# Optimization experiments

Measured on AMD Instinct MI355X. Metric: run time of the kernel, lower is better.

Reference implementation:

```python
import jax, jax.numpy as jnp
import numpy as np
from jax.scipy.special import logsumexp

L, B, T = 512, 512, 128


def setup_inputs() -> dict:
    key = jax.random.key(0)
    k0, k1, k2, k3, k4 = jax.random.split(key, 5)
    emissions = jax.random.normal(k0, (L, B, T), dtype=jnp.float32)
    tags = jax.random.randint(k1, (L, B), 0, T)
    mask = jnp.ones((L, B), dtype=bool)
    u = lambda k, s: jax.random.uniform(k, s, jnp.float32, -0.1, 0.1)
    return {
        "emissions": emissions,
        "tags": tags,
        "mask": mask,
        "start_transitions": u(k2, (T,)),
        "end_transitions": u(k3, (T,)),
        "transitions": u(k4, (T, T)),
    }


def reference(emissions, tags, mask, start_transitions, end_transitions, transitions):
    # emissions: (L, B, T) float; tags: (L, B) int; mask: (L, B) bool
    seq_len, batch, n_tag = emissions.shape

    # ---- numerator: score of the gold tag sequence (summed over batch) ----
    # per-step emission score at the gold tag
    step_scores = jnp.take_along_axis(emissions, tags[:, :, None], axis=2)[:, :, 0]  # (L, B)
    # transition score tags[i-1] -> tags[i] for i >= 1
    trans_scores = transitions[tags[:-1], tags[1:]]  # (L-1, B)
    scores = step_scores.at[1:].add(trans_scores)
    log_numerator = jnp.sum(jnp.where(mask, scores, jnp.float32(0.0)))
    ends = mask.sum(axis=0) - 1  # (B,) last valid index per sequence
    log_numerator += start_transitions[tags[0]].sum()
    last_tags = jnp.take_along_axis(tags, ends[None, :], axis=0)[0]  # (B,)
    log_numerator += end_transitions[last_tags].sum()

    # ---- denominator: log partition via forward algorithm (lax.scan over time) ----
    alpha0 = start_transitions + emissions[0]  # (B, T)

    def step(alpha, xs):
        emit_i, mask_i = xs  # (B, T), (B,)
        # scores[b, s, t] = alpha[b, s] + transitions[s, t] + emit_i[b, t]
        scores = alpha[:, :, None] + transitions[None, :, :] + emit_i[:, None, :]
        new_alpha = logsumexp(scores, axis=1)  # (B, T)
        alpha = jnp.where(mask_i[:, None], new_alpha, alpha)
        return alpha, None

    alpha, _ = jax.lax.scan(step, alpha0, (emissions[1:], mask[1:]))
    log_denominator = logsumexp(alpha + end_transitions, axis=1).sum()

    return (log_denominator - log_numerator) / batch
```

## Files before the change

### kernel.cpp

```cpp
#include <hip/hip_runtime.h>

#define L_SEQ 512
#define BATCH 512
#define NTAG  128
#define LOG2E 1.44269504088896340736f
#define LN2_D 0.69314718055994530942

typedef _Float16 h2 __attribute__((ext_vector_type(2)));
typedef _Float16 h8 __attribute__((ext_vector_type(8)));


__global__ void k_init(const float* __restrict__ trans, h2* __restrict__ ctp,
                       int* __restrict__ counter) {
    int g = blockIdx.x * blockDim.x + threadIdx.x;
    if (g < NTAG * 64) {
        int j = g >> 6, t = g & 63;
        h2 v;
        v[0] = (_Float16)__expf(trans[(2 * t)     * NTAG + j]);
        v[1] = (_Float16)__expf(trans[(2 * t + 1) * NTAG + j]);
        ctp[g] = v;
    }
    if (g == 0) *counter = 0;
}

#define Q16(F) F(0) F(1) F(2) F(3) F(4) F(5) F(6) F(7) \
               F(8) F(9) F(10) F(11) F(12) F(13) F(14) F(15)

#define DECL_C(n) h8 c##n = colp[n];

#define DOTG(n) { h8 qv = q8[n]; \
  s0 = __builtin_amdgcn_fdot2(__builtin_shufflevector(qv, qv, 0, 1), \
                              __builtin_shufflevector(c##n, c##n, 0, 1), s0, false); \
  s1 = __builtin_amdgcn_fdot2(__builtin_shufflevector(qv, qv, 2, 3), \
                              __builtin_shufflevector(c##n, c##n, 2, 3), s1, false); \
  s2 = __builtin_amdgcn_fdot2(__builtin_shufflevector(qv, qv, 4, 5), \
                              __builtin_shufflevector(c##n, c##n, 4, 5), s2, false); \
  s3 = __builtin_amdgcn_fdot2(__builtin_shufflevector(qv, qv, 6, 7), \
                              __builtin_shufflevector(c##n, c##n, 6, 7), s3, false); }

__global__ void __launch_bounds__(128, 1)
k_main(const float* __restrict__ emissions,
       const int* __restrict__ tags,
       const float* __restrict__ start_t,
       const float* __restrict__ end_t,
       const float* __restrict__ trans,
       const h2* __restrict__ ctp,
       float* __restrict__ ws_val,
       int* __restrict__ counter,
       float* __restrict__ out) {
    const int b = blockIdx.x;
    const int j = threadIdx.x;
    const int wave = j >> 6;
    const int lane = j & 63;

    __shared__ __align__(16) _Float16 q_h[2][136];
    __shared__ float D_sh[2];
    __shared__ float red_sh[2];
    __shared__ int   s_last;

    float num = 0.f;
    #pragma unroll
    for (int l = j; l < L_SEQ; l += 128) {
        int tag = tags[l * BATCH + b];
        float sc = emissions[((size_t)l * BATCH + b) * NTAG + tag];
        if (l > 0) {
            int prev = tags[(l - 1) * BATCH + b];
            sc += trans[prev * NTAG + tag];
        } else {
            sc += start_t[tag];
        }
        if (l == L_SEQ - 1) sc += end_t[tag];
        num += sc;
    }
    #pragma unroll
    for (int off = 32; off; off >>= 1) num += __shfl_xor(num, off, 64);
    if (lane == 0) red_sh[wave] = num;

    const h8* colp = (const h8*)(ctp + (size_t)j * 64);
    Q16(DECL_C)

    __syncthreads();
    const float num_b = red_sh[0] + red_sh[1];

    const float ee = __expf(end_t[j]);
    float alpha0 = start_t[j] + emissions[(size_t)b * NTAG + j];
    float q_own = exp2f(alpha0 * LOG2E);
    double C = 0.0;

    float m0 = alpha0;
    #pragma unroll
    for (int off = 32; off; off >>= 1) m0 = fmaxf(m0, __shfl_xor(m0, off, 64));
    __syncthreads();
    if (lane == 0) red_sh[wave] = m0;
    __syncthreads();
    float D_stash = fmaxf(red_sh[0], red_sh[1]) * LOG2E + 13.5f;

    const size_t STRIDE = (size_t)BATCH * NTAG;
    const float* em_base = emissions + (size_t)b * NTAG + j;
    float em_cur = em_base[1 * STRIDE];
    float em_n1  = em_base[2 * STRIDE];
    float em_n2  = em_base[3 * STRIDE];

    for (int l = 1; l < L_SEQ; ++l) {
        const int p = l & 1;
        q_h[p][j] = (_Float16)fminf(q_own, 60000.f);
        if (j == 0) D_sh[p] = D_stash;
        int pf = l + 3; if (pf > L_SEQ - 1) pf = L_SEQ - 1;
        float em_pf = em_base[(size_t)pf * STRIDE];

        __syncthreads();
        const h8* q8 = (const h8*)q_h[p];
        float D_f = D_sh[p];

        float s0 = 0.f, s1 = 0.f, s2 = 0.f, s3 = 0.f;
        Q16(DOTG)

        float S = (s0 + s1) + (s2 + s3);
        if (j == 0)
            D_stash = fmaf(0.5f, __log2f(fmaxf(S, 1e-30f)),
                           fmaf(0.3f, D_f, 6.5f));
        q_own = S * exp2f(fmaf(em_cur, LOG2E, -D_f));
        C += (double)D_f * LN2_D;

        em_cur = em_n1; em_n1 = em_n2; em_n2 = em_pf;
    }

    float wv = q_own * ee;
    #pragma unroll
    for (int off = 32; off; off >>= 1) wv += __shfl_xor(wv, off, 64);
    __syncthreads();
    if (lane == 0) red_sh[wave] = wv;
    __syncthreads();
    float tot = red_sh[0] + red_sh[1];
    float val = (float)(C + (double)__logf(tot)) - num_b;

    if (j == 0) {
        __hip_atomic_store(&ws_val[b], val, __ATOMIC_RELAXED, __HIP_MEMORY_SCOPE_AGENT);
        __threadfence();
        int old = atomicAdd(counter, 1);
        s_last = (old == (int)gridDim.x - 1) ? 1 : 0;
    }
    __syncthreads();
    if (s_last) {
        __threadfence();
        float acc = 0.f;
        #pragma unroll
        for (int t = j; t < BATCH; t += 128)
            acc += __hip_atomic_load(&ws_val[t], __ATOMIC_RELAXED, __HIP_MEMORY_SCOPE_AGENT);
        #pragma unroll
        for (int off = 32; off; off >>= 1) acc += __shfl_xor(acc, off, 64);
        if (lane == 0) red_sh[wave] = acc;
        __syncthreads();
        if (j == 0) out[0] = (red_sh[0] + red_sh[1]) / (float)BATCH;
    }
}

extern "C" void kernel_launch(void* const* d_in, const int* in_sizes, int n_in,
                              void* d_out, int out_size, void* d_ws, size_t ws_size,
                              hipStream_t stream) {
    const float* emissions = (const float*)d_in[0];
    const int*   tags      = (const int*)d_in[1];
    const float* start_t   = (const float*)d_in[3];
    const float* end_t     = (const float*)d_in[4];
    const float* trans     = (const float*)d_in[5];

    char*  wsb     = (char*)d_ws;
    h2*    ctp     = (h2*)wsb;
    float* ws_val  = (float*)(wsb + 32768);
    int*   counter = (int*)(wsb + 32768 + 2048);
    float* out     = (float*)d_out;

    k_init<<<(NTAG * 64 + 255) / 256, 256, 0, stream>>>(trans, ctp, counter);
    k_main<<<BATCH, NTAG, 0, stream>>>(emissions, tags, start_t, end_t, trans, ctp,
                                       ws_val, counter, out);
}
```

Measured before the change: 438.6 us.

## Split each tag's transition dot product across four threads per block

Raises the block from 128 to 512 threads and gives each tag a quad of threads. Each thread holds a quarter of the transition column and does 16 fdot2 instead of 64, then the quad combines its partial sums with two cross-lane shuffles. This shortens the per-step critical path of the serial forward recurrence, which is latency-bound with only 2 waves per block. The cost is redundant emission loads and exp work in each quad, two extra shuffles per step, and reductions over 8 waves instead of 2.

After: 439.2 us. About the same (+0.1%).

```diff
diff --git a/kernel.cpp b/kernel.cpp
--- a/kernel.cpp
+++ b/kernel.cpp
@@ -3,6 +3,7 @@
 #define L_SEQ 512
 #define BATCH 512
 #define NTAG  128
+#define NTHR  512
 #define LOG2E 1.44269504088896340736f
 #define LN2_D 0.69314718055994530942
 
@@ -23,22 +24,17 @@
     if (g == 0) *counter = 0;
 }
 
-#define Q16(F) F(0) F(1) F(2) F(3) F(4) F(5) F(6) F(7) \
-               F(8) F(9) F(10) F(11) F(12) F(13) F(14) F(15)
+#define DOTG(cn, n) { h8 qv = q8[qbase + n]; \
+  s0 = __builtin_amdgcn_fdot2(__builtin_shufflevector(qv, qv, 0, 1), \
+                              __builtin_shufflevector(cn, cn, 0, 1), s0, false); \
+  s1 = __builtin_amdgcn_fdot2(__builtin_shufflevector(qv, qv, 2, 3), \
+                              __builtin_shufflevector(cn, cn, 2, 3), s1, false); \
+  s2 = __builtin_amdgcn_fdot2(__builtin_shufflevector(qv, qv, 4, 5), \
+                              __builtin_shufflevector(cn, cn, 4, 5), s2, false); \
+  s3 = __builtin_amdgcn_fdot2(__builtin_shufflevector(qv, qv, 6, 7), \
+                              __builtin_shufflevector(cn, cn, 6, 7), s3, false); }
 
-#define DECL_C(n) h8 c##n = colp[n];
-
-#define DOTG(n) { h8 qv = q8[n]; \
-  s0 = __builtin_amdgcn_fdot2(__builtin_shufflevector(qv, qv, 0, 1), \
-                              __builtin_shufflevector(c##n, c##n, 0, 1), s0, false); \
-  s1 = __builtin_amdgcn_fdot2(__builtin_shufflevector(qv, qv, 2, 3), \
-                              __builtin_shufflevector(c##n, c##n, 2, 3), s1, false); \
-  s2 = __builtin_amdgcn_fdot2(__builtin_shufflevector(qv, qv, 4, 5), \
-                              __builtin_shufflevector(c##n, c##n, 4, 5), s2, false); \
-  s3 = __builtin_amdgcn_fdot2(__builtin_shufflevector(qv, qv, 6, 7), \
-                              __builtin_shufflevector(c##n, c##n, 6, 7), s3, false); }
-
-__global__ void __launch_bounds__(128, 1)
+__global__ void __launch_bounds__(NTHR, 4)
 k_main(const float* __restrict__ emissions,
        const int* __restrict__ tags,
        const float* __restrict__ start_t,
@@ -48,19 +44,21 @@
        float* __restrict__ ws_val,
        int* __restrict__ counter,
        float* __restrict__ out) {
-    const int b = blockIdx.x;
-    const int j = threadIdx.x;
-    const int wave = j >> 6;
-    const int lane = j & 63;
+    const int b    = blockIdx.x;
+    const int t    = threadIdx.x;
+    const int j    = t >> 2;
+    const int qh   = t & 3;
+    const int wave = t >> 6;
+    const int lane = t & 63;
 
-    __shared__ __align__(16) _Float16 q_h[2][136];
+    __shared__ __align__(16) _Float16 q_h[2][NTAG];
     __shared__ float D_sh[2];
-    __shared__ float red_sh[2];
+    __shared__ float red_sh[8];
     __shared__ int   s_last;
 
-    float num = 0.f;
-    #pragma unroll
-    for (int l = j; l < L_SEQ; l += 128) {
+    float num;
+    {
+        const int l = t;
         int tag = tags[l * BATCH + b];
         float sc = emissions[((size_t)l * BATCH + b) * NTAG + tag];
         if (l > 0) {
@@ -70,17 +68,23 @@
             sc += start_t[tag];
         }
         if (l == L_SEQ - 1) sc += end_t[tag];
-        num += sc;
+        num = sc;
     }
     #pragma unroll
     for (int off = 32; off; off >>= 1) num += __shfl_xor(num, off, 64);
     if (lane == 0) red_sh[wave] = num;
 
+    const int qbase = qh * 4;
     const h8* colp = (const h8*)(ctp + (size_t)j * 64);
-    Q16(DECL_C)
+    h8 c0 = colp[qbase + 0];
+    h8 c1 = colp[qbase + 1];
+    h8 c2 = colp[qbase + 2];
+    h8 c3 = colp[qbase + 3];
 
     __syncthreads();
-    const float num_b = red_sh[0] + red_sh[1];
+    float num_b = 0.f;
+    #pragma unroll
+    for (int w = 0; w < 8; ++w) num_b += red_sh[w];
 
     const float ee = __expf(end_t[j]);
     float alpha0 = start_t[j] + emissions[(size_t)b * NTAG + j];
@@ -93,7 +97,10 @@
     __syncthreads();
     if (lane == 0) red_sh[wave] = m0;
     __syncthreads();
-    float D_stash = fmaxf(red_sh[0], red_sh[1]) * LOG2E + 13.5f;
+    float mx = red_sh[0];
+    #pragma unroll
+    for (int w = 1; w < 8; ++w) mx = fmaxf(mx, red_sh[w]);
+    float D_stash = mx * LOG2E + 13.5f;
 
     const size_t STRIDE = (size_t)BATCH * NTAG;
     const float* em_base = emissions + (size_t)b * NTAG + j;
@@ -103,8 +110,8 @@
 
     for (int l = 1; l < L_SEQ; ++l) {
         const int p = l & 1;
-        q_h[p][j] = (_Float16)fminf(q_own, 60000.f);
-        if (j == 0) D_sh[p] = D_stash;
+        if (qh == 0) q_h[p][j] = (_Float16)fminf(q_own, 60000.f);
+        if (t == 0)  D_sh[p] = D_stash;
         int pf = l + 3; if (pf > L_SEQ - 1) pf = L_SEQ - 1;
         float em_pf = em_base[(size_t)pf * STRIDE];
 
@@ -113,10 +120,13 @@
         float D_f = D_sh[p];
 
         float s0 = 0.f, s1 = 0.f, s2 = 0.f, s3 = 0.f;
-        Q16(DOTG)
+        DOTG(c0, 0) DOTG(c1, 1) DOTG(c2, 2) DOTG(c3, 3)
 
         float S = (s0 + s1) + (s2 + s3);
-        if (j == 0)
+        S += __shfl_xor(S, 1, 64);
+        S += __shfl_xor(S, 2, 64);
+
+        if (t == 0)
             D_stash = fmaf(0.5f, __log2f(fmaxf(S, 1e-30f)),
                            fmaf(0.3f, D_f, 6.5f));
         q_own = S * exp2f(fmaf(em_cur, LOG2E, -D_f));
@@ -125,16 +135,18 @@
         em_cur = em_n1; em_n1 = em_n2; em_n2 = em_pf;
     }
 
-    float wv = q_own * ee;
+    float wv = (qh == 0) ? q_own * ee : 0.f;
     #pragma unroll
     for (int off = 32; off; off >>= 1) wv += __shfl_xor(wv, off, 64);
     __syncthreads();
     if (lane == 0) red_sh[wave] = wv;
     __syncthreads();
-    float tot = red_sh[0] + red_sh[1];
+    float tot = 0.f;
+    #pragma unroll
+    for (int w = 0; w < 8; ++w) tot += red_sh[w];
     float val = (float)(C + (double)__logf(tot)) - num_b;
 
-    if (j == 0) {
+    if (t == 0) {
         __hip_atomic_store(&ws_val[b], val, __ATOMIC_RELAXED, __HIP_MEMORY_SCOPE_AGENT);
         __threadfence();
         int old = atomicAdd(counter, 1);
@@ -143,15 +155,18 @@
     __syncthreads();
     if (s_last) {
         __threadfence();
-        float acc = 0.f;
-        #pragma unroll
-        for (int t = j; t < BATCH; t += 128)
-            acc += __hip_atomic_load(&ws_val[t], __ATOMIC_RELAXED, __HIP_MEMORY_SCOPE_AGENT);
+        float acc = __hip_atomic_load(&ws_val[t], __ATOMIC_RELAXED,
+                                      __HIP_MEMORY_SCOPE_AGENT);
         #pragma unroll
         for (int off = 32; off; off >>= 1) acc += __shfl_xor(acc, off, 64);
         if (lane == 0) red_sh[wave] = acc;
         __syncthreads();
-        if (j == 0) out[0] = (red_sh[0] + red_sh[1]) / (float)BATCH;
+        if (t == 0) {
+            float a = 0.f;
+            #pragma unroll
+            for (int w = 0; w < 8; ++w) a += red_sh[w];
+            out[0] = a / (float)BATCH;
+        }
     }
 }
 
@@ -171,6 +186,6 @@
     float* out     = (float*)d_out;
 
     k_init<<<(NTAG * 64 + 255) / 256, 256, 0, stream>>>(trans, ctp, counter);
-    k_main<<<BATCH, NTAG, 0, stream>>>(emissions, tags, start_t, end_t, trans, ctp,
+    k_main<<<BATCH, NTHR, 0, stream>>>(emissions, tags, start_t, end_t, trans, ctp,
                                        ws_val, counter, out);
 }
```

## Run forward recursion in a single wave using readlane broadcast instead of LDS

Applied to the files above, without the earlier changes.

Each batch sequence now runs in one 64-lane wavefront that owns two tags per lane, and the transition matrix is repacked so lane j holds the columns for tags j and j+64. The per-step alpha vector is packed as fp16 pairs and broadcast with readlane instead of going through shared memory. This removes the per-step __syncthreads and LDS traffic, and the scale factor D is computed redundantly on every lane rather than passed through shared memory. In exchange each lane does twice the dot-product work and holds twice the transition registers, and there are half as many threads per CU.

Result: no change. 435.8 us (-0.6%).

```diff
diff --git a/kernel.cpp b/kernel.cpp
--- a/kernel.cpp
+++ b/kernel.cpp
@@ -16,8 +16,8 @@
     if (g < NTAG * 64) {
         int j = g >> 6, t = g & 63;
         h2 v;
-        v[0] = (_Float16)__expf(trans[(2 * t)     * NTAG + j]);
-        v[1] = (_Float16)__expf(trans[(2 * t + 1) * NTAG + j]);
+        v[0] = (_Float16)__expf(trans[t * NTAG + j]);
+        v[1] = (_Float16)__expf(trans[(t + 64) * NTAG + j]);
         ctp[g] = v;
     }
     if (g == 0) *counter = 0;
@@ -26,19 +26,27 @@
 #define Q16(F) F(0) F(1) F(2) F(3) F(4) F(5) F(6) F(7) \
                F(8) F(9) F(10) F(11) F(12) F(13) F(14) F(15)
 
-#define DECL_C(n) h8 c##n = colp[n];
+#define DECL_C(n) h8 cA##n = colA[n]; h8 cB##n = colB[n];
 
-#define DOTG(n) { h8 qv = q8[n]; \
-  s0 = __builtin_amdgcn_fdot2(__builtin_shufflevector(qv, qv, 0, 1), \
-                              __builtin_shufflevector(c##n, c##n, 0, 1), s0, false); \
-  s1 = __builtin_amdgcn_fdot2(__builtin_shufflevector(qv, qv, 2, 3), \
-                              __builtin_shufflevector(c##n, c##n, 2, 3), s1, false); \
-  s2 = __builtin_amdgcn_fdot2(__builtin_shufflevector(qv, qv, 4, 5), \
-                              __builtin_shufflevector(c##n, c##n, 4, 5), s2, false); \
-  s3 = __builtin_amdgcn_fdot2(__builtin_shufflevector(qv, qv, 6, 7), \
-                              __builtin_shufflevector(c##n, c##n, 6, 7), s3, false); }
+#define CHUNK(c) { \
+    int r0 = __builtin_amdgcn_readlane(qpk_i, 4*(c)+0); \
+    int r1 = __builtin_amdgcn_readlane(qpk_i, 4*(c)+1); \
+    int r2 = __builtin_amdgcn_readlane(qpk_i, 4*(c)+2); \
+    int r3 = __builtin_amdgcn_readlane(qpk_i, 4*(c)+3); \
+    h2 b0 = __builtin_bit_cast(h2, r0); \
+    h2 b1 = __builtin_bit_cast(h2, r1); \
+    h2 b2 = __builtin_bit_cast(h2, r2); \
+    h2 b3 = __builtin_bit_cast(h2, r3); \
+    sA0 = __builtin_amdgcn_fdot2(b0, __builtin_shufflevector(cA##c, cA##c, 0, 1), sA0, false); \
+    sA1 = __builtin_amdgcn_fdot2(b1, __builtin_shufflevector(cA##c, cA##c, 2, 3), sA1, false); \
+    sA2 = __builtin_amdgcn_fdot2(b2, __builtin_shufflevector(cA##c, cA##c, 4, 5), sA2, false); \
+    sA3 = __builtin_amdgcn_fdot2(b3, __builtin_shufflevector(cA##c, cA##c, 6, 7), sA3, false); \
+    sB0 = __builtin_amdgcn_fdot2(b0, __builtin_shufflevector(cB##c, cB##c, 0, 1), sB0, false); \
+    sB1 = __builtin_amdgcn_fdot2(b1, __builtin_shufflevector(cB##c, cB##c, 2, 3), sB1, false); \
+    sB2 = __builtin_amdgcn_fdot2(b2, __builtin_shufflevector(cB##c, cB##c, 4, 5), sB2, false); \
+    sB3 = __builtin_amdgcn_fdot2(b3, __builtin_shufflevector(cB##c, cB##c, 6, 7), sB3, false); }
 
-__global__ void __launch_bounds__(128, 1)
+__global__ void __launch_bounds__(64, 1)
 k_main(const float* __restrict__ emissions,
        const int* __restrict__ tags,
        const float* __restrict__ start_t,
@@ -48,19 +56,14 @@
        float* __restrict__ ws_val,
        int* __restrict__ counter,
        float* __restrict__ out) {
-    const int b = blockIdx.x;
-    const int j = threadIdx.x;
-    const int wave = j >> 6;
-    const int lane = j & 63;
-
-    __shared__ __align__(16) _Float16 q_h[2][136];
-    __shared__ float D_sh[2];
-    __shared__ float red_sh[2];
-    __shared__ int   s_last;
+    const int b    = blockIdx.x;
+    const int lane = threadIdx.x;
+    const int j    = lane;
 
     float num = 0.f;
     #pragma unroll
-    for (int l = j; l < L_SEQ; l += 128) {
+    for (int k = 0; k < L_SEQ / 64; ++k) {
+        const int l = lane + 64 * k;
         int tag = tags[l * BATCH + b];
         float sc = emissions[((size_t)l * BATCH + b) * NTAG + tag];
         if (l > 0) {
@@ -74,84 +77,89 @@
     }
     #pragma unroll
     for (int off = 32; off; off >>= 1) num += __shfl_xor(num, off, 64);
-    if (lane == 0) red_sh[wave] = num;
+    const float num_b = num;
 
-    const h8* colp = (const h8*)(ctp + (size_t)j * 64);
+    const h8* colA = (const h8*)(ctp + (size_t)j * 64);
+    const h8* colB = (const h8*)(ctp + (size_t)(j + 64) * 64);
     Q16(DECL_C)
 
-    __syncthreads();
-    const float num_b = red_sh[0] + red_sh[1];
-
-    const float ee = __expf(end_t[j]);
-    float alpha0 = start_t[j] + emissions[(size_t)b * NTAG + j];
-    float q_own = exp2f(alpha0 * LOG2E);
+    const float eeA = __expf(end_t[j]);
+    const float eeB = __expf(end_t[j + 64]);
+    float a0A = start_t[j]      + emissions[(size_t)b * NTAG + j];
+    float a0B = start_t[j + 64] + emissions[(size_t)b * NTAG + j + 64];
+    float q_A = exp2f(a0A * LOG2E);
+    float q_B = exp2f(a0B * LOG2E);
     double C = 0.0;
 
-    float m0 = alpha0;
+    float m0 = fmaxf(a0A, a0B);
     #pragma unroll
     for (int off = 32; off; off >>= 1) m0 = fmaxf(m0, __shfl_xor(m0, off, 64));
-    __syncthreads();
-    if (lane == 0) red_sh[wave] = m0;
-    __syncthreads();
-    float D_stash = fmaxf(red_sh[0], red_sh[1]) * LOG2E + 13.5f;
+    float D_f = m0 * LOG2E + 13.5f;
 
     const size_t STRIDE = (size_t)BATCH * NTAG;
-    const float* em_base = emissions + (size_t)b * NTAG + j;
-    float em_cur = em_base[1 * STRIDE];
-    float em_n1  = em_base[2 * STRIDE];
-    float em_n2  = em_base[3 * STRIDE];
+    const float* em_baseA = emissions + (size_t)b * NTAG + j;
+    const float* em_baseB = em_baseA + 64;
+    float emA_cur = em_baseA[1 * STRIDE];
+    float emA_n1  = em_baseA[2 * STRIDE];
+    float emA_n2  = em_baseA[3 * STRIDE];
+    float emB_cur = em_baseB[1 * STRIDE];
+    float emB_n1  = em_baseB[2 * STRIDE];
+    float emB_n2  = em_baseB[3 * STRIDE];
 
     for (int l = 1; l < L_SEQ; ++l) {
-        const int p = l & 1;
-        q_h[p][j] = (_Float16)fminf(q_own, 60000.f);
-        if (j == 0) D_sh[p] = D_stash;
+        h2 qpk;
+        qpk[0] = (_Float16)fminf(q_A, 60000.f);
+        qpk[1] = (_Float16)fminf(q_B, 60000.f);
+        int qpk_i = __builtin_bit_cast(int, qpk);
+
         int pf = l + 3; if (pf > L_SEQ - 1) pf = L_SEQ - 1;
-        float em_pf = em_base[(size_t)pf * STRIDE];
+        float pfA = em_baseA[(size_t)pf * STRIDE];
+        float pfB = em_baseB[(size_t)pf * STRIDE];
 
-        __syncthreads();
-        const h8* q8 = (const h8*)q_h[p];
-        float D_f = D_sh[p];
+        float sA0 = 0.f, sA1 = 0.f, sA2 = 0.f, sA3 = 0.f;
+        float sB0 = 0.f, sB1 = 0.f, sB2 = 0.f, sB3 = 0.f;
+        Q16(CHUNK)
 
-        float s0 = 0.f, s1 = 0.f, s2 = 0.f, s3 = 0.f;
-        Q16(DOTG)
+        float SA = (sA0 + sA1) + (sA2 + sA3);
+        float SB = (sB0 + sB1) + (sB2 + sB3);
 
-        float S = (s0 + s1) + (s2 + s3);
-        if (j == 0)
-            D_stash = fmaf(0.5f, __log2f(fmaxf(S, 1e-30f)),
-                           fmaf(0.3f, D_f, 6.5f));
-        q_own = S * exp2f(fmaf(em_cur, LOG2E, -D_f));
+        int s0i = __builtin_amdgcn_readfirstlane(__builtin_bit_cast(int, SA));
+        float S0 = __builtin_bit_cast(float, s0i);
+        float D_next = fmaf(0.5f, __log2f(fmaxf(S0, 1e-30f)),
+                            fmaf(0.3f, D_f, 6.5f));
+
+        q_A = SA * exp2f(fmaf(emA_cur, LOG2E, -D_f));
+        q_B = SB * exp2f(fmaf(emB_cur, LOG2E, -D_f));
         C += (double)D_f * LN2_D;
+        D_f = D_next;
 
-        em_cur = em_n1; em_n1 = em_n2; em_n2 = em_pf;
+        emA_cur = emA_n1; emA_n1 = emA_n2; emA_n2 = pfA;
+        emB_cur = emB_n1; emB_n1 = emB_n2; emB_n2 = pfB;
     }
 
-    float wv = q_own * ee;
+    float wv = q_A * eeA + q_B * eeB;
     #pragma unroll
     for (int off = 32; off; off >>= 1) wv += __shfl_xor(wv, off, 64);
-    __syncthreads();
-    if (lane == 0) red_sh[wave] = wv;
-    __syncthreads();
-    float tot = red_sh[0] + red_sh[1];
-    float val = (float)(C + (double)__logf(tot)) - num_b;
+    float val = (float)(C + (double)__logf(wv)) - num_b;
 
-    if (j == 0) {
+    int last = 0;
+    if (lane == 0) {
         __hip_atomic_store(&ws_val[b], val, __ATOMIC_RELAXED, __HIP_MEMORY_SCOPE_AGENT);
         __threadfence();
         int old = atomicAdd(counter, 1);
-        s_last = (old == (int)gridDim.x - 1) ? 1 : 0;
+        last = (old == (int)gridDim.x - 1) ? 1 : 0;
     }
-    __syncthreads();
-    if (s_last) {
+    last = __builtin_amdgcn_readlane(last, 0);
+    if (last) {
         __threadfence();
         float acc = 0.f;
         #pragma unroll
-        for (int t = j; t < BATCH; t += 128)
-            acc += __hip_atomic_load(&ws_val[t], __ATOMIC_RELAXED, __HIP_MEMORY_SCOPE_AGENT);
+        for (int k = 0; k < BATCH / 64; ++k)
+            acc += __hip_atomic_load(&ws_val[lane + 64 * k], __ATOMIC_RELAXED,
+                                     __HIP_MEMORY_SCOPE_AGENT);
         #pragma unroll
         for (int off = 32; off; off >>= 1) acc += __shfl_xor(acc, off, 64);
-        if (lane == 0) red_sh[wave] = acc;
-        __syncthreads();
-        if (j == 0) out[0] = (red_sh[0] + red_sh[1]) / (float)BATCH;
+        if (lane == 0) out[0] = acc / (float)BATCH;
     }
 }
 
@@ -171,6 +179,6 @@
     float* out     = (float*)d_out;
 
     k_init<<<(NTAG * 64 + 255) / 256, 256, 0, stream>>>(trans, ctp, counter);
-    k_main<<<BATCH, NTAG, 0, stream>>>(emissions, tags, start_t, end_t, trans, ctp,
-                                       ws_val, counter, out);
+    k_main<<<BATCH, 64, 0, stream>>>(emissions, tags, start_t, end_t, trans, ctp,
+                                     ws_val, counter, out);
 }
```

## Batch 16 sequences per wave and run forward recursion on MFMA tiles

Applied to the files above, without the earlier changes.

The forward algorithm is recast as a matrix product in which each 64-thread block processes 16 batch sequences. Each step runs a chain of 16x16x32 f16 MFMA instructions against an exp-transition table held in LDS, replacing the per-sequence fdot2 dot products and the per-step __syncthreads. The gold-path numerator and the swizzled transition table now come from the init kernel. Emission loads are vectorized and triple-buffered in registers. Only 32 blocks are launched, which leaves most CUs idle and makes each step latency-bound on the serial MFMA chain.

Result: slower. 950.1 us (+116.6%).

```diff
diff --git a/kernel.cpp b/kernel.cpp
--- a/kernel.cpp
+++ b/kernel.cpp
@@ -5,62 +5,30 @@
 #define NTAG  128
 #define LOG2E 1.44269504088896340736f
 #define LN2_D 0.69314718055994530942
-
-typedef _Float16 h2 __attribute__((ext_vector_type(2)));
-typedef _Float16 h8 __attribute__((ext_vector_type(8)));
-
-
-__global__ void k_init(const float* __restrict__ trans, h2* __restrict__ ctp,
+#define ESTR  (BATCH * NTAG)
+
+typedef _Float16 h2   __attribute__((ext_vector_type(2)));
+typedef _Float16 h8   __attribute__((ext_vector_type(8)));
+typedef float    f32x4 __attribute__((ext_vector_type(4)));
+
+
+__global__ void k_init(const float* __restrict__ emissions,
+                       const int* __restrict__ tags,
+                       const float* __restrict__ start_t,
+                       const float* __restrict__ end_t,
+                       const float* __restrict__ trans,
+                       h2* __restrict__ atab,
+                       float* __restrict__ ws_num,
                        int* __restrict__ counter) {
-    int g = blockIdx.x * blockDim.x + threadIdx.x;
-    if (g < NTAG * 64) {
-        int j = g >> 6, t = g & 63;
-        h2 v;
-        v[0] = (_Float16)__expf(trans[(2 * t)     * NTAG + j]);
-        v[1] = (_Float16)__expf(trans[(2 * t + 1) * NTAG + j]);
-        ctp[g] = v;
-    }
-    if (g == 0) *counter = 0;
-}
-
-#define Q16(F) F(0) F(1) F(2) F(3) F(4) F(5) F(6) F(7) \
-               F(8) F(9) F(10) F(11) F(12) F(13) F(14) F(15)
-
-#define DECL_C(n) h8 c##n = colp[n];
-
-#define DOTG(n) { h8 qv = q8[n]; \
-  s0 = __builtin_amdgcn_fdot2(__builtin_shufflevector(qv, qv, 0, 1), \
-                              __builtin_shufflevector(c##n, c##n, 0, 1), s0, false); \
-  s1 = __builtin_amdgcn_fdot2(__builtin_shufflevector(qv, qv, 2, 3), \
-                              __builtin_shufflevector(c##n, c##n, 2, 3), s1, false); \
-  s2 = __builtin_amdgcn_fdot2(__builtin_shufflevector(qv, qv, 4, 5), \
-                              __builtin_shufflevector(c##n, c##n, 4, 5), s2, false); \
-  s3 = __builtin_amdgcn_fdot2(__builtin_shufflevector(qv, qv, 6, 7), \
-                              __builtin_shufflevector(c##n, c##n, 6, 7), s3, false); }
-
-__global__ void __launch_bounds__(128, 1)
-k_main(const float* __restrict__ emissions,
-       const int* __restrict__ tags,
-       const float* __restrict__ start_t,
-       const float* __restrict__ end_t,
-       const float* __restrict__ trans,
-       const h2* __restrict__ ctp,
-       float* __restrict__ ws_val,
-       int* __restrict__ counter,
-       float* __restrict__ out) {
     const int b = blockIdx.x;
-    const int j = threadIdx.x;
-    const int wave = j >> 6;
-    const int lane = j & 63;
-
-    __shared__ __align__(16) _Float16 q_h[2][136];
-    __shared__ float D_sh[2];
+    const int t = threadIdx.x;
+    const int wave = t >> 6, lane = t & 63;
     __shared__ float red_sh[2];
-    __shared__ int   s_last;
 
     float num = 0.f;
     #pragma unroll
-    for (int l = j; l < L_SEQ; l += 128) {
+    for (int k = 0; k < L_SEQ / 128; ++k) {
+        const int l = t + 128 * k;
         int tag = tags[l * BATCH + b];
         float sc = emissions[((size_t)l * BATCH + b) * NTAG + tag];
         if (l > 0) {
@@ -75,83 +43,203 @@
     #pragma unroll
     for (int off = 32; off; off >>= 1) num += __shfl_xor(num, off, 64);
     if (lane == 0) red_sh[wave] = num;
-
-    const h8* colp = (const h8*)(ctp + (size_t)j * 64);
-    Q16(DECL_C)
-
     __syncthreads();
-    const float num_b = red_sh[0] + red_sh[1];
-
-    const float ee = __expf(end_t[j]);
-    float alpha0 = start_t[j] + emissions[(size_t)b * NTAG + j];
-    float q_own = exp2f(alpha0 * LOG2E);
+    if (t == 0) ws_num[b] = red_sh[0] + red_sh[1];
+
+    int gid = b * 128 + t;
+    if (gid < 8192) {
+        int f   = gid >> 8;
+        int rem = gid & 255;
+        int ln  = rem >> 2;
+        int d   = rem & 3;
+        int r = f >> 2, c = f & 3;
+        int i = ln & 15, kg = ln >> 4;
+        int tn  = 32 * (r >> 1) + 8 * (i >> 2) + 4 * (r & 1) + (i & 3);
+        int tp  = 32 * c + 8 * kg + 2 * d;
+        h2 v;
+        v[0] = (_Float16)__expf(trans[tp * NTAG + tn]);
+        v[1] = (_Float16)__expf(trans[(tp + 1) * NTAG + tn]);
+        atab[gid] = v;
+    }
+    if (gid == 0) *counter = 0;
+}
+
+#define MF(A, B, Cc) __builtin_amdgcn_mfma_f32_16x16x32_f16((A), (B), (Cc), 0, 0, 0)
+
+#define TILES \
+    unsigned abase_ = (unsigned)(l64 * 16); \
+    asm volatile("" : "+v"(abase_)); \
+    const char* AB_ = (const char*)Alds + abase_; \
+    const f32x4 z_ = {0.f, 0.f, 0.f, 0.f}; \
+    f32x4 s0 = MF(*(const h8*)(AB_ +  0*1024), B0, z_); \
+    s0 = MF(*(const h8*)(AB_ +  1*1024), B1, s0); \
+    s0 = MF(*(const h8*)(AB_ +  2*1024), B2, s0); \
+    s0 = MF(*(const h8*)(AB_ +  3*1024), B3, s0); \
+    f32x4 s1 = MF(*(const h8*)(AB_ +  4*1024), B0, z_); \
+    s1 = MF(*(const h8*)(AB_ +  5*1024), B1, s1); \
+    s1 = MF(*(const h8*)(AB_ +  6*1024), B2, s1); \
+    s1 = MF(*(const h8*)(AB_ +  7*1024), B3, s1); \
+    f32x4 s2 = MF(*(const h8*)(AB_ +  8*1024), B0, z_); \
+    s2 = MF(*(const h8*)(AB_ +  9*1024), B1, s2); \
+    s2 = MF(*(const h8*)(AB_ + 10*1024), B2, s2); \
+    s2 = MF(*(const h8*)(AB_ + 11*1024), B3, s2); \
+    f32x4 s3 = MF(*(const h8*)(AB_ + 12*1024), B0, z_); \
+    s3 = MF(*(const h8*)(AB_ + 13*1024), B1, s3); \
+    s3 = MF(*(const h8*)(AB_ + 14*1024), B2, s3); \
+    s3 = MF(*(const h8*)(AB_ + 15*1024), B3, s3); \
+    f32x4 s4 = MF(*(const h8*)(AB_ + 16*1024), B0, z_); \
+    s4 = MF(*(const h8*)(AB_ + 17*1024), B1, s4); \
+    s4 = MF(*(const h8*)(AB_ + 18*1024), B2, s4); \
+    s4 = MF(*(const h8*)(AB_ + 19*1024), B3, s4); \
+    f32x4 s5 = MF(*(const h8*)(AB_ + 20*1024), B0, z_); \
+    s5 = MF(*(const h8*)(AB_ + 21*1024), B1, s5); \
+    s5 = MF(*(const h8*)(AB_ + 22*1024), B2, s5); \
+    s5 = MF(*(const h8*)(AB_ + 23*1024), B3, s5); \
+    f32x4 s6 = MF(*(const h8*)(AB_ + 24*1024), B0, z_); \
+    s6 = MF(*(const h8*)(AB_ + 25*1024), B1, s6); \
+    s6 = MF(*(const h8*)(AB_ + 26*1024), B2, s6); \
+    s6 = MF(*(const h8*)(AB_ + 27*1024), B3, s6); \
+    f32x4 s7 = MF(*(const h8*)(AB_ + 28*1024), B0, z_); \
+    s7 = MF(*(const h8*)(AB_ + 29*1024), B1, s7); \
+    s7 = MF(*(const h8*)(AB_ + 30*1024), B2, s7); \
+    s7 = MF(*(const h8*)(AB_ + 31*1024), B3, s7);
+
+#define REPACK(SA, SB, EA, EB, BV) { \
+    float qa0 = fminf(SA[0] * exp2f(fmaf(EA[0], LOG2E, -D_f)), 60000.f); \
+    float qa1 = fminf(SA[1] * exp2f(fmaf(EA[1], LOG2E, -D_f)), 60000.f); \
+    float qa2 = fminf(SA[2] * exp2f(fmaf(EA[2], LOG2E, -D_f)), 60000.f); \
+    float qa3 = fminf(SA[3] * exp2f(fmaf(EA[3], LOG2E, -D_f)), 60000.f); \
+    float qb0 = fminf(SB[0] * exp2f(fmaf(EB[0], LOG2E, -D_f)), 60000.f); \
+    float qb1 = fminf(SB[1] * exp2f(fmaf(EB[1], LOG2E, -D_f)), 60000.f); \
+    float qb2 = fminf(SB[2] * exp2f(fmaf(EB[2], LOG2E, -D_f)), 60000.f); \
+    float qb3 = fminf(SB[3] * exp2f(fmaf(EB[3], LOG2E, -D_f)), 60000.f); \
+    h8 bv_; \
+    bv_[0]=(_Float16)qa0; bv_[1]=(_Float16)qa1; bv_[2]=(_Float16)qa2; bv_[3]=(_Float16)qa3; \
+    bv_[4]=(_Float16)qb0; bv_[5]=(_Float16)qb1; bv_[6]=(_Float16)qb2; bv_[7]=(_Float16)qb3; \
+    BV = bv_; }
+
+#define LOADALL(E, L) { \
+    int lc_ = (L); if (lc_ > L_SEQ - 1) lc_ = L_SEQ - 1; \
+    const float* ep_ = emP + (size_t)lc_ * ESTR; \
+    E##0 = *(const f32x4*)(ep_ +   0); E##1 = *(const f32x4*)(ep_ +   4); \
+    E##2 = *(const f32x4*)(ep_ +  32); E##3 = *(const f32x4*)(ep_ +  36); \
+    E##4 = *(const f32x4*)(ep_ +  64); E##5 = *(const f32x4*)(ep_ +  68); \
+    E##6 = *(const f32x4*)(ep_ +  96); E##7 = *(const f32x4*)(ep_ + 100); }
+
+#define STEP(E, PFL) do { \
+    TILES; \
+    int s00i_ = __builtin_amdgcn_ds_bpermute(col * 4, __builtin_bit_cast(int, s0[0])); \
+    float Dn_ = fmaf(0.5f, __log2f(fmaxf(__builtin_bit_cast(float, s00i_), 1e-30f)), \
+                     fmaf(0.3f, D_f, 6.5f)); \
+    REPACK(s0, s1, E##0, E##1, B0); \
+    REPACK(s2, s3, E##2, E##3, B1); \
+    REPACK(s4, s5, E##4, E##5, B2); \
+    REPACK(s6, s7, E##6, E##7, B3); \
+    C += (double)D_f * LN2_D; D_f = Dn_; \
+    LOADALL(E, PFL); \
+} while (0)
+
+#define INITC(c, BV) { \
+    const float* e_  = emb + 32*(c) + 8*g; \
+    const float* st_ = start_t + 32*(c) + 8*g; \
+    f32x4 e0_ = *(const f32x4*)(e_);      f32x4 e1_ = *(const f32x4*)(e_ + 4); \
+    f32x4 t0_ = *(const f32x4*)(st_);     f32x4 t1_ = *(const f32x4*)(st_ + 4); \
+    float a0_=e0_[0]+t0_[0], a1_=e0_[1]+t0_[1], a2_=e0_[2]+t0_[2], a3_=e0_[3]+t0_[3]; \
+    float a4_=e1_[0]+t1_[0], a5_=e1_[1]+t1_[1], a6_=e1_[2]+t1_[2], a7_=e1_[3]+t1_[3]; \
+    m0 = fmaxf(m0, fmaxf(fmaxf(fmaxf(a0_,a1_),fmaxf(a2_,a3_)), \
+                         fmaxf(fmaxf(a4_,a5_),fmaxf(a6_,a7_)))); \
+    h8 bv_; \
+    bv_[0]=(_Float16)fminf(exp2f(a0_*LOG2E),60000.f); \
+    bv_[1]=(_Float16)fminf(exp2f(a1_*LOG2E),60000.f); \
+    bv_[2]=(_Float16)fminf(exp2f(a2_*LOG2E),60000.f); \
+    bv_[3]=(_Float16)fminf(exp2f(a3_*LOG2E),60000.f); \
+    bv_[4]=(_Float16)fminf(exp2f(a4_*LOG2E),60000.f); \
+    bv_[5]=(_Float16)fminf(exp2f(a5_*LOG2E),60000.f); \
+    bv_[6]=(_Float16)fminf(exp2f(a6_*LOG2E),60000.f); \
+    bv_[7]=(_Float16)fminf(exp2f(a7_*LOG2E),60000.f); \
+    BV = bv_; }
+
+#define FINR(S, EA, OFFC) { \
+    f32x4 ev_ = *(const f32x4*)(endP + (OFFC)); \
+    wv += S[0]*exp2f(fmaf(EA[0],LOG2E,-D_f)) * __expf(ev_[0]); \
+    wv += S[1]*exp2f(fmaf(EA[1],LOG2E,-D_f)) * __expf(ev_[1]); \
+    wv += S[2]*exp2f(fmaf(EA[2],LOG2E,-D_f)) * __expf(ev_[2]); \
+    wv += S[3]*exp2f(fmaf(EA[3],LOG2E,-D_f)) * __expf(ev_[3]); }
+
+__global__ void
+__attribute__((amdgpu_flat_work_group_size(64, 64), amdgpu_waves_per_eu(1, 1)))
+k_main(const float* __restrict__ emissions,
+       const float* __restrict__ start_t,
+       const float* __restrict__ end_t,
+       const h2* __restrict__ atab,
+       const float* __restrict__ ws_num,
+       float* __restrict__ ws_val,
+       int* __restrict__ counter,
+       float* __restrict__ out) {
+    const int l64 = threadIdx.x;
+    const int g   = l64 >> 4;
+    const int col = l64 & 15;
+    const int b   = blockIdx.x * 16 + col;
+
+    __shared__ __align__(16) h8 Alds[2048];
+
+    const h8* gt = (const h8*)atab;
+    #pragma unroll
+    for (int f = 0; f < 32; ++f) Alds[f * 64 + l64] = gt[f * 64 + l64];
+    __syncthreads();
+
+    const float* emb = emissions + (size_t)b * NTAG;
+    float m0 = -1e30f;
+    h8 B0, B1, B2, B3;
+    INITC(0, B0) INITC(1, B1) INITC(2, B2) INITC(3, B3)
+    m0 = fmaxf(m0, __shfl_xor(m0, 16, 64));
+    m0 = fmaxf(m0, __shfl_xor(m0, 32, 64));
+    float D_f = m0 * LOG2E + 13.5f;
     double C = 0.0;
 
-    float m0 = alpha0;
-    #pragma unroll
-    for (int off = 32; off; off >>= 1) m0 = fmaxf(m0, __shfl_xor(m0, off, 64));
-    __syncthreads();
-    if (lane == 0) red_sh[wave] = m0;
-    __syncthreads();
-    float D_stash = fmaxf(red_sh[0], red_sh[1]) * LOG2E + 13.5f;
-
-    const size_t STRIDE = (size_t)BATCH * NTAG;
-    const float* em_base = emissions + (size_t)b * NTAG + j;
-    float em_cur = em_base[1 * STRIDE];
-    float em_n1  = em_base[2 * STRIDE];
-    float em_n2  = em_base[3 * STRIDE];
-
-    for (int l = 1; l < L_SEQ; ++l) {
-        const int p = l & 1;
-        q_h[p][j] = (_Float16)fminf(q_own, 60000.f);
-        if (j == 0) D_sh[p] = D_stash;
-        int pf = l + 3; if (pf > L_SEQ - 1) pf = L_SEQ - 1;
-        float em_pf = em_base[(size_t)pf * STRIDE];
-
-        __syncthreads();
-        const h8* q8 = (const h8*)q_h[p];
-        float D_f = D_sh[p];
-
-        float s0 = 0.f, s1 = 0.f, s2 = 0.f, s3 = 0.f;
-        Q16(DOTG)
-
-        float S = (s0 + s1) + (s2 + s3);
-        if (j == 0)
-            D_stash = fmaf(0.5f, __log2f(fmaxf(S, 1e-30f)),
-                           fmaf(0.3f, D_f, 6.5f));
-        q_own = S * exp2f(fmaf(em_cur, LOG2E, -D_f));
+    const float* emP = emissions + (size_t)b * NTAG + 8 * g;
+    f32x4 P0, P1, P2, P3, P4, P5, P6, P7;
+    f32x4 Q0, Q1, Q2, Q3, Q4, Q5, Q6, Q7;
+    f32x4 R0, R1, R2, R3, R4, R5, R6, R7;
+    LOADALL(P, 1); LOADALL(Q, 2); LOADALL(R, 3);
+
+    for (int l = 1; l <= 508; l += 3) {
+        STEP(P, l + 3);
+        STEP(Q, l + 4);
+        STEP(R, l + 5);
+    }
+
+    {
+        TILES;
         C += (double)D_f * LN2_D;
-
-        em_cur = em_n1; em_n1 = em_n2; em_n2 = em_pf;
-    }
-
-    float wv = q_own * ee;
-    #pragma unroll
-    for (int off = 32; off; off >>= 1) wv += __shfl_xor(wv, off, 64);
-    __syncthreads();
-    if (lane == 0) red_sh[wave] = wv;
-    __syncthreads();
-    float tot = red_sh[0] + red_sh[1];
-    float val = (float)(C + (double)__logf(tot)) - num_b;
-
-    if (j == 0) {
-        __hip_atomic_store(&ws_val[b], val, __ATOMIC_RELAXED, __HIP_MEMORY_SCOPE_AGENT);
+        const float* endP = end_t + 8 * g;
+        float wv = 0.f;
+        FINR(s0, P0,   0) FINR(s1, P1,   4) FINR(s2, P2,  32) FINR(s3, P3,  36)
+        FINR(s4, P4,  64) FINR(s5, P5,  68) FINR(s6, P6,  96) FINR(s7, P7, 100)
+        wv += __shfl_xor(wv, 16, 64);
+        wv += __shfl_xor(wv, 32, 64);
+        float val = (float)(C + (double)__logf(wv)) - ws_num[b];
+        if (l64 < 16)
+            __hip_atomic_store(&ws_val[b], val, __ATOMIC_RELAXED,
+                               __HIP_MEMORY_SCOPE_AGENT);
+    }
+
+    int last = 0;
+    if (l64 == 0) {
         __threadfence();
-        int old = atomicAdd(counter, 1);
-        s_last = (old == (int)gridDim.x - 1) ? 1 : 0;
-    }
-    __syncthreads();
-    if (s_last) {
+        last = (atomicAdd(counter, 1) == (int)gridDim.x - 1) ? 1 : 0;
+    }
+    last = __builtin_amdgcn_readlane(last, 0);
+    if (last) {
         __threadfence();
         float acc = 0.f;
         #pragma unroll
-        for (int t = j; t < BATCH; t += 128)
-            acc += __hip_atomic_load(&ws_val[t], __ATOMIC_RELAXED, __HIP_MEMORY_SCOPE_AGENT);
+        for (int k = 0; k < BATCH / 64; ++k)
+            acc += __hip_atomic_load(&ws_val[l64 + 64 * k], __ATOMIC_RELAXED,
+                                     __HIP_MEMORY_SCOPE_AGENT);
         #pragma unroll
         for (int off = 32; off; off >>= 1) acc += __shfl_xor(acc, off, 64);
-        if (lane == 0) red_sh[wave] = acc;
-        __syncthreads();
-        if (j == 0) out[0] = (red_sh[0] + red_sh[1]) / (float)BATCH;
+        if (l64 == 0) out[0] = acc / (float)BATCH;
     }
 }
 
@@ -165,12 +253,14 @@
     const float* trans     = (const float*)d_in[5];
 
     char*  wsb     = (char*)d_ws;
-    h2*    ctp     = (h2*)wsb;
-    float* ws_val  = (float*)(wsb + 32768);
-    int*   counter = (int*)(wsb + 32768 + 2048);
+    h2*    atab    = (h2*)wsb;
+    float* ws_num  = (float*)(wsb + 32768);
+    float* ws_val  = (float*)(wsb + 32768 + 2048);
+    int*   counter = (int*)(wsb + 32768 + 4096);
     float* out     = (float*)d_out;
 
-    k_init<<<(NTAG * 64 + 255) / 256, 256, 0, stream>>>(trans, ctp, counter);
-    k_main<<<BATCH, NTAG, 0, stream>>>(emissions, tags, start_t, end_t, trans, ctp,
-                                       ws_val, counter, out);
+    k_init<<<BATCH, 128, 0, stream>>>(emissions, tags, start_t, end_t, trans,
+                                      atab, ws_num, counter);
+    k_main<<<32, 64, 0, stream>>>(emissions, start_t, end_t, atab, ws_num,
+                                  ws_val, counter, out);
 }
```
